# Kernel tuning notes

Measured on AMD Instinct MI355X. Metric: run time of the kernel, lower is better.

Reference implementation:

```python
import jax, jax.numpy as jnp
import numpy as np

N_ATOMS = 50000
N_EDGES = 100000
ATOM_DIM = 64
BOND_DIM = 16


def setup_inputs() -> dict:
    key = jax.random.key(0)
    k1, k2, k3, k4 = jax.random.split(key, 4)
    atom_features = jax.random.normal(k1, (N_ATOMS, ATOM_DIM), dtype=jnp.float32)
    bond_features = jax.random.normal(k2, (N_EDGES, BOND_DIM), dtype=jnp.float32)
    pair_indices = jax.random.randint(k3, (N_EDGES, 2), 0, N_ATOMS, dtype=jnp.int32)
    kernel = jax.random.normal(k4, (BOND_DIM, ATOM_DIM * ATOM_DIM), dtype=jnp.float32) * (1.0 / np.sqrt(BOND_DIM))
    bias = jnp.zeros((ATOM_DIM * ATOM_DIM,), dtype=jnp.float32)
    return {"atom_features": atom_features, "bond_features": bond_features,
            "pair_indices": pair_indices, "kernel": kernel, "bias": bias}


def reference(atom_features, bond_features, pair_indices, kernel, bias):
    n_atoms, d = atom_features.shape
    # per-edge learned linear transform: [E, bond_dim] @ [bond_dim, d*d] -> [E, d, d]
    edge_mats = (bond_features @ kernel + bias).reshape(-1, d, d)
    # gather neighbor atom features (axis 0)
    neighbors = atom_features[pair_indices[:, 1]]  # [E, d]
    # batched matvec: [E, d, d] x [E, d] -> [E, d]
    transformed = jnp.einsum('eij,ej->ei', edge_mats, neighbors)
    # scatter-add to source atoms (true segment_sum, no one-hot materialization)
    aggregated = jax.ops.segment_sum(transformed, pair_indices[:, 0], num_segments=n_atoms)
    return aggregated
```

## Files before the change

### kernel.cpp

```cpp
#include <hip/hip_runtime.h>
#include <hip/hip_bf16.h>


#define N_EDGES   100000
#define DIM       64
#define BDIM      16
#define TILE      32
#define NTILES    (N_EDGES / TILE)
#define BLOCK     512
#define GRID      256
#define NKS       20

#define NB_OFF(p)        ((p) * 8192)
#define BOND_OFF(p)      (16384 + (p) * 2560)
#define SRC_OFF(p)       (21504 + (p) * 128)
#define COMB_OFF(p,h,qq) (21760 + ((((p)*2+(h))*3)+(qq)) * 4096)
#define LDS_TOTAL        70912

typedef __bf16 bf16x8 __attribute__((ext_vector_type(8)));
typedef float  f32x16 __attribute__((ext_vector_type(16)));

__global__ __launch_bounds__(BLOCK, 2)
void edge_mfma_kernel(const float* __restrict__ atom,
                      const float* __restrict__ bondf,
                      const int*   __restrict__ pair,
                      const float* __restrict__ kmat,
                      const float* __restrict__ bias,
                      float* __restrict__ out)
{
    extern __shared__ char smem[];
    const int tid = threadIdx.x;
    const int l   = tid & 63;
    const int wid = tid >> 6;
    const int q   = wid >> 1;
    const int h   = wid & 1;
    const int ma  = l & 31;
    const int hi  = l >> 5;
    const int n   = h * 32 + (l & 31);

    bf16x8 wfr[NKS];
    #pragma unroll
    for (int ci = 0; ci < 5; ++ci) {
        const int c = q * 5 + ci;
        #pragma unroll
        for (int ss = 0; ss < 4; ++ss) {
            bf16x8 w;
            if (c < 17) {
                const float* src = (c < BDIM) ? (kmat + c * (DIM * DIM) + n * DIM + ss * 16 + hi * 8)
                                              : (bias + n * DIM + ss * 16 + hi * 8);
                float4 v0 = *(const float4*)(src);
                float4 v1 = *(const float4*)(src + 4);
                w[0] = (__bf16)v0.x; w[1] = (__bf16)v0.y; w[2] = (__bf16)v0.z; w[3] = (__bf16)v0.w;
                w[4] = (__bf16)v1.x; w[5] = (__bf16)v1.y; w[6] = (__bf16)v1.z; w[7] = (__bf16)v1.w;
            } else {
                #pragma unroll
                for (int j = 0; j < 8; ++j) w[j] = (__bf16)0.0f;
            }
            wfr[ci * 4 + ss] = w;
        }
    }

    auto stage = [&](int stile, int pbuf) {
        const int sm = tid >> 4, sp = tid & 15;
        const int e  = stile * TILE + sm;
        const int dst = pair[2 * e + 1];
        float4 v = *(const float4*)(atom + dst * DIM + sp * 4);
        float* nbb = (float*)(smem + NB_OFF(pbuf));
        *(float4*)(nbb + sm * 64 + ((sp ^ (sm & 7)) << 2)) = v;
        float* bb = (float*)(smem + BOND_OFF(pbuf));
        bb[sm * 20 + sp] = bondf[e * BDIM + sp];
        if (sp == 0) {
            bb[sm * 20 + 16] = 1.0f;
            ((int*)(smem + SRC_OFF(pbuf)))[sm] = pair[2 * e];
        } else if (sp < 4) {
            bb[sm * 20 + 16 + sp] = 0.0f;
        }
    };

    int tile = blockIdx.x;
    stage(tile, 0);
    __syncthreads();
    int p = 0;

    while (true) {
        const int  ntile = tile + GRID;
        const bool more  = (ntile < NTILES);
        if (more) stage(ntile, p ^ 1);

        const float* nbb = (const float*)(smem + NB_OFF(p));
        const float* bb  = (const float*)(smem + BOND_OFF(p));

        float nbf[32];
        #pragma unroll
        for (int ss = 0; ss < 4; ++ss) {
            const int cb = ss * 4 + hi * 2;
            float4 u0 = *(const float4*)(nbb + ma * 64 + (((cb    ) ^ (ma & 7)) << 2));
            float4 u1 = *(const float4*)(nbb + ma * 64 + (((cb + 1) ^ (ma & 7)) << 2));
            nbf[ss*8+0] = u0.x; nbf[ss*8+1] = u0.y; nbf[ss*8+2] = u0.z; nbf[ss*8+3] = u0.w;
            nbf[ss*8+4] = u1.x; nbf[ss*8+5] = u1.y; nbf[ss*8+6] = u1.z; nbf[ss*8+7] = u1.w;
        }
        float bnd[5];
        #pragma unroll
        for (int ci = 0; ci < 5; ++ci) bnd[ci] = bb[ma * 20 + q * 5 + ci];

        f32x16 ac0, ac1;
        #pragma unroll
        for (int i = 0; i < 16; ++i) { ac0[i] = 0.0f; ac1[i] = 0.0f; }

        #pragma unroll
        for (int ks = 0; ks < NKS; ++ks) {
            const int ci = ks >> 2, ss = ks & 3;
            const float bv = bnd[ci];
            bf16x8 a;
            a[0] = (__bf16)(bv * nbf[ss*8+0]); a[1] = (__bf16)(bv * nbf[ss*8+1]);
            a[2] = (__bf16)(bv * nbf[ss*8+2]); a[3] = (__bf16)(bv * nbf[ss*8+3]);
            a[4] = (__bf16)(bv * nbf[ss*8+4]); a[5] = (__bf16)(bv * nbf[ss*8+5]);
            a[6] = (__bf16)(bv * nbf[ss*8+6]); a[7] = (__bf16)(bv * nbf[ss*8+7]);
            if (ks & 1) ac1 = __builtin_amdgcn_mfma_f32_32x32x16_bf16(a, wfr[ks], ac1, 0, 0, 0);
            else        ac0 = __builtin_amdgcn_mfma_f32_32x32x16_bf16(a, wfr[ks], ac0, 0, 0, 0);
        }
        #pragma unroll
        for (int r = 0; r < 16; ++r) ac0[r] += ac1[r];

        int oaddr[16];
        if (q == 0) {
            const int* sr = (const int*)(smem + SRC_OFF(p));
            #pragma unroll
            for (int r = 0; r < 16; ++r) {
                const int m = (r & 3) + 8 * (r >> 2) + 4 * hi;
                oaddr[r] = sr[m] * DIM + n;
            }
        } else {
            float* cbw = (float*)(smem + COMB_OFF(p, h, q - 1));
            #pragma unroll
            for (int r = 0; r < 16; ++r) cbw[r * 64 + l] = ac0[r];
        }

        __syncthreads();

        if (q == 0) {
            const float* c0 = (const float*)(smem + COMB_OFF(p, h, 0));
            const float* c1 = (const float*)(smem + COMB_OFF(p, h, 1));
            const float* c2 = (const float*)(smem + COMB_OFF(p, h, 2));
            #pragma unroll
            for (int r = 0; r < 16; ++r)
                atomicAdd(out + oaddr[r], ac0[r] + c0[r*64+l] + c1[r*64+l] + c2[r*64+l]);
        }
        if (!more) break;
        tile = ntile; p ^= 1;
    }
}

extern "C" void kernel_launch(void* const* d_in, const int* in_sizes, int n_in,
                              void* d_out, int out_size, void* d_ws, size_t ws_size,
                              hipStream_t stream)
{
    const float* atom  = (const float*)d_in[0];
    const float* bondf = (const float*)d_in[1];
    const int*   pair  = (const int*)  d_in[2];
    const float* kmat  = (const float*)d_in[3];
    const float* bias  = (const float*)d_in[4];
    float* out = (float*)d_out;

    hipFuncSetAttribute((const void*)edge_mfma_kernel,
                        hipFuncAttributeMaxDynamicSharedMemorySize, LDS_TOTAL);
    hipMemsetAsync(out, 0, (size_t)out_size * sizeof(float), stream);
    edge_mfma_kernel<<<GRID, BLOCK, LDS_TOTAL, stream>>>(atom, bondf, pair, kmat, bias, out);
}
```

Before: 122.5 us.

## Replace atomic scatter-add with linked-list gather over materialized per-edge outputs

The MFMA edge kernel now writes per-edge transformed vectors to a workspace buffer instead of issuing float atomics into the output. A build kernel constructs per-atom linked lists of incoming edges via atomicExch, and a gather kernel walks each atom's list to sum its edge rows and writes the output directly, which also removes the output memset. This trades the atomic contention for a 25.6 MB intermediate write and read, two extra launches, and serial pointer-chasing per atom. The old atomic path is kept as a fallback when the workspace is too small.

New measurement: 133.6 us. 9.1% more time.

```diff
diff --git a/kernel.cpp b/kernel.cpp
--- a/kernel.cpp
+++ b/kernel.cpp
@@ -2,6 +2,7 @@
 #include <hip/hip_bf16.h>
 
 
+#define N_ATOMS   50000
 #define N_EDGES   100000
 #define DIM       64
 #define BDIM      16
@@ -20,13 +21,11 @@
 typedef __bf16 bf16x8 __attribute__((ext_vector_type(8)));
 typedef float  f32x16 __attribute__((ext_vector_type(16)));
 
-__global__ __launch_bounds__(BLOCK, 2)
-void edge_mfma_kernel(const float* __restrict__ atom,
-                      const float* __restrict__ bondf,
-                      const int*   __restrict__ pair,
-                      const float* __restrict__ kmat,
-                      const float* __restrict__ bias,
-                      float* __restrict__ out)
+template <int EPI>
+__device__ __forceinline__
+void edge_body(const float* __restrict__ atom, const float* __restrict__ bondf,
+               const int* __restrict__ pair, const float* __restrict__ kmat,
+               const float* __restrict__ bias, float* __restrict__ dstbuf)
 {
     extern __shared__ char smem[];
     const int tid = threadIdx.x;
@@ -71,7 +70,7 @@
         bb[sm * 20 + sp] = bondf[e * BDIM + sp];
         if (sp == 0) {
             bb[sm * 20 + 16] = 1.0f;
-            ((int*)(smem + SRC_OFF(pbuf)))[sm] = pair[2 * e];
+            if (EPI == 1) ((int*)(smem + SRC_OFF(pbuf)))[sm] = pair[2 * e];
         } else if (sp < 4) {
             bb[sm * 20 + 16 + sp] = 0.0f;
         }
@@ -124,11 +123,13 @@
 
         int oaddr[16];
         if (q == 0) {
-            const int* sr = (const int*)(smem + SRC_OFF(p));
-            #pragma unroll
-            for (int r = 0; r < 16; ++r) {
-                const int m = (r & 3) + 8 * (r >> 2) + 4 * hi;
-                oaddr[r] = sr[m] * DIM + n;
+            if (EPI == 1) {
+                const int* sr = (const int*)(smem + SRC_OFF(p));
+                #pragma unroll
+                for (int r = 0; r < 16; ++r) {
+                    const int m = (r & 3) + 8 * (r >> 2) + 4 * hi;
+                    oaddr[r] = sr[m] * DIM + n;
+                }
             }
         } else {
             float* cbw = (float*)(smem + COMB_OFF(p, h, q - 1));
@@ -143,12 +144,54 @@
             const float* c1 = (const float*)(smem + COMB_OFF(p, h, 1));
             const float* c2 = (const float*)(smem + COMB_OFF(p, h, 2));
             #pragma unroll
-            for (int r = 0; r < 16; ++r)
-                atomicAdd(out + oaddr[r], ac0[r] + c0[r*64+l] + c1[r*64+l] + c2[r*64+l]);
+            for (int r = 0; r < 16; ++r) {
+                const float val = ac0[r] + c0[r*64+l] + c1[r*64+l] + c2[r*64+l];
+                if (EPI == 0) {
+                    const int m = (r & 3) + 8 * (r >> 2) + 4 * hi;
+                    dstbuf[(size_t)(tile * TILE + m) * DIM + n] = val;
+                } else {
+                    atomicAdd(dstbuf + oaddr[r], val);
+                }
+            }
         }
         if (!more) break;
         tile = ntile; p ^= 1;
     }
+}
+
+__global__ __launch_bounds__(BLOCK, 2)
+void edge_transform_kernel(const float* __restrict__ atom, const float* __restrict__ bondf,
+                           const int* __restrict__ pair, const float* __restrict__ kmat,
+                           const float* __restrict__ bias, float* __restrict__ tr)
+{ edge_body<0>(atom, bondf, pair, kmat, bias, tr); }
+
+__global__ __launch_bounds__(BLOCK, 2)
+void edge_atomic_kernel(const float* __restrict__ atom, const float* __restrict__ bondf,
+                        const int* __restrict__ pair, const float* __restrict__ kmat,
+                        const float* __restrict__ bias, float* __restrict__ out)
+{ edge_body<1>(atom, bondf, pair, kmat, bias, out); }
+
+__global__ __launch_bounds__(256)
+void build_kernel(const int* __restrict__ pair, int* __restrict__ head, int* __restrict__ nxt)
+{
+    const int e = blockIdx.x * 256 + threadIdx.x;
+    if (e < N_EDGES)
+        nxt[e] = atomicExch(&head[pair[2 * e]], e);
+}
+
+__global__ __launch_bounds__(256)
+void gather_kernel(const int* __restrict__ head, const int* __restrict__ nxt,
+                   const float* __restrict__ tr, float* __restrict__ out)
+{
+    const int a = blockIdx.x * 4 + (threadIdx.x >> 6);
+    const int l = threadIdx.x & 63;
+    float acc = 0.0f;
+    int e = head[a];
+    while (e >= 0) {
+        acc += tr[(size_t)e * DIM + l];
+        e = nxt[e];
+    }
+    out[(size_t)a * DIM + l] = acc;
 }
 
 extern "C" void kernel_launch(void* const* d_in, const int* in_sizes, int n_in,
@@ -162,8 +205,26 @@
     const float* bias  = (const float*)d_in[4];
     float* out = (float*)d_out;
 
-    hipFuncSetAttribute((const void*)edge_mfma_kernel,
-                        hipFuncAttributeMaxDynamicSharedMemorySize, LDS_TOTAL);
-    hipMemsetAsync(out, 0, (size_t)out_size * sizeof(float), stream);
-    edge_mfma_kernel<<<GRID, BLOCK, LDS_TOTAL, stream>>>(atom, bondf, pair, kmat, bias, out);
-}
+    const size_t tr_bytes   = (size_t)N_EDGES * DIM * sizeof(float);
+    const size_t head_bytes = (size_t)N_ATOMS * sizeof(int);
+    const size_t nxt_bytes  = (size_t)N_EDGES * sizeof(int);
+    const size_t need = tr_bytes + head_bytes + nxt_bytes;
+
+    if (ws_size >= need) {
+        float* tr  = (float*)d_ws;
+        int* head  = (int*)((char*)d_ws + tr_bytes);
+        int* nxt   = head + N_ATOMS;
+
+        hipFuncSetAttribute((const void*)edge_transform_kernel,
+                            hipFuncAttributeMaxDynamicSharedMemorySize, LDS_TOTAL);
+        hipMemsetAsync(head, 0xFF, head_bytes, stream);
+        build_kernel<<<(N_EDGES + 255) / 256, 256, 0, stream>>>(pair, head, nxt);
+        edge_transform_kernel<<<GRID, BLOCK, LDS_TOTAL, stream>>>(atom, bondf, pair, kmat, bias, tr);
+        gather_kernel<<<N_ATOMS / 4, 256, 0, stream>>>(head, nxt, tr, out);
+    } else {
+        hipFuncSetAttribute((const void*)edge_atomic_kernel,
+                            hipFuncAttributeMaxDynamicSharedMemorySize, LDS_TOTAL);
+        hipMemsetAsync(out, 0, (size_t)out_size * sizeof(float), stream);
+        edge_atomic_kernel<<<GRID, BLOCK, LDS_TOTAL, stream>>>(atom, bondf, pair, kmat, bias, out);
+    }
+}
```
